# Kernel tuning notes

Hardware: AMD Instinct MI355X
Metric: run time of the kernel (lower is better)

The kernel has to match this reference:

```python
import jax, jax.numpy as jnp
import numpy as np

B, T, W, E, H, EMB, NVOCAB, WIN = 256, 200, 200, 768, 256, 32, 201, 8


def setup_inputs() -> dict:
    key = jax.random.key(0)
    ks = jax.random.split(key, 12)
    s = 0.05
    inputs = jax.random.normal(ks[0], (B, T, E), jnp.float32)
    full_word_embeddings = jax.random.normal(ks[1], (B, W, E), jnp.float32)
    lengths = jax.random.randint(ks[2], (B,), T // 2, T + 1)
    fix = jax.random.randint(ks[3], (B, T), 1, NVOCAB)
    fix_seq = jnp.where(jnp.arange(T)[None, :] < lengths[:, None], fix, 0)
    emb_table = (jax.random.normal(ks[4], (NVOCAB, EMB)) * s).at[0].set(0.0)  # padding_idx=0
    W_ih = jax.random.normal(ks[5], (3 * H, E + EMB)) * s  # torch GRU layout, gates r,z,n
    W_hh = jax.random.normal(ks[6], (3 * H, H)) * s
    b_ih = jax.random.normal(ks[7], (3 * H,)) * s
    b_hh = jax.random.normal(ks[8], (3 * H,)) * s
    W_out = jax.random.normal(ks[9], (E, H)) * s  # output_layer: Linear(H, E)
    b_out = jnp.zeros((E,), jnp.float32)
    W_dur = jax.random.normal(ks[10], (1, H)) * s  # duration_layer: Linear(H, 1)
    b_dur = jnp.zeros((1,), jnp.float32)
    return {"inputs": inputs, "fix_seq": fix_seq, "full_word_embeddings": full_word_embeddings,
            "lengths": lengths, "expert_id": 0, "emb_table": emb_table,
            "W_ih": W_ih, "b_ih": b_ih, "W_hh": W_hh, "b_hh": b_hh,
            "W_out": W_out, "b_out": b_out, "W_dur": W_dur, "b_dur": b_dur}


def _gru(x, W_ih, b_ih, W_hh, b_hh, h_dim):
    # x: [B,T,I]. Precompute input projections once, scan over time.
    xg = jnp.einsum('bti,gi->btg', x, W_ih) + b_ih  # [B,T,3H]

    def step(h, xg_t):
        hg = h @ W_hh.T + b_hh
        xr, xz, xn = jnp.split(xg_t, 3, axis=-1)
        hr, hz, hn = jnp.split(hg, 3, axis=-1)
        r = jax.nn.sigmoid(xr + hr)
        z = jax.nn.sigmoid(xz + hz)
        n = jnp.tanh(xn + r * hn)
        h_new = (1.0 - z) * n + z * h
        return h_new, h_new

    h0 = jnp.zeros((x.shape[0], h_dim), x.dtype)
    _, outs = jax.lax.scan(step, h0, jnp.swapaxes(xg, 0, 1))
    return jnp.swapaxes(outs, 0, 1)  # [B,T,H]


def reference(inputs, fix_seq, full_word_embeddings, lengths, expert_id,
              emb_table, W_ih, b_ih, W_hh, b_hh, W_out, b_out, W_dur, b_dur):
    del expert_id  # weights of the selected expert are passed directly
    valid_mask = fix_seq != 0
    scan_emb = emb_table[fix_seq]  # [B,T,32]
    rnn_in = jnp.concatenate([inputs, scan_emb], axis=-1)
    outputs = _gru(rnn_in, W_ih, b_ih, W_hh, b_hh, W_hh.shape[1])  # [B,T,H]
    # pad_packed_sequence zeros outputs beyond each sequence length
    tmask = jnp.arange(outputs.shape[1])[None, :] < lengths[:, None]
    outputs = outputs * tmask[..., None].astype(outputs.dtype)
    # dot attention: proj then scores against word embeddings
    proj = outputs @ W_out.T + b_out  # [B,T,E]
    logits = jnp.einsum('bte,bwe->btw', proj, full_word_embeddings)
    # saccade window mask around current fixation position
    wpos = jnp.arange(full_word_embeddings.shape[1])[None, None, :]
    dist = jnp.abs(wpos - fix_seq[..., None])
    sacc = (dist <= WIN) & valid_mask[..., None]
    logits = jnp.where(sacc, logits, -1e9)
    word_mask = jnp.sum(jnp.abs(full_word_embeddings), axis=-1) != 0
    logits = jnp.where(word_mask[:, None, :], logits, -1e9)
    dur_pred = (outputs @ W_dur.T + b_dur)[..., 0]  # [B,T]
    return logits, dur_pred
```

## Files before the change

kernel.cpp:

```cpp
#include <hip/hip_runtime.h>
#include <hip/hip_bf16.h>

typedef __attribute__((ext_vector_type(8))) short bf16x8;
typedef __attribute__((ext_vector_type(4))) float f32x4;
typedef __attribute__((ext_vector_type(4))) int   i32x4;

#define NB 256
#define NT 200
#define NW 200
#define NE 768
#define NH 256
#define NEMB 32
#define KIN 800
#define G3H 768
#define MROWS 51200

__device__ __forceinline__ float bf2f(unsigned short h) {
    return __uint_as_float(((unsigned)h) << 16);
}
__device__ __forceinline__ unsigned short f2bf(float f) {
    unsigned u = __float_as_uint(f);
    u += 0x7fff + ((u >> 16) & 1);
    return (unsigned short)(u >> 16);
}
__device__ __forceinline__ float sigm(float x) { return 1.0f / (1.0f + __expf(-x)); }
__device__ __forceinline__ float tanh_fast(float x) {
    float e = __expf(2.0f * x);
    return 1.0f - 2.0f / (e + 1.0f);
}

#if __has_builtin(__builtin_amdgcn_sdot4)
__device__ __forceinline__ int SDOT4(int a, int b, int c) {
    return __builtin_amdgcn_sdot4(a, b, c, false);
}
#else
__device__ __forceinline__ int SDOT4(int a, int b, int c) {
    #pragma unroll
    for (int j = 0; j < 4; j++)
        c += (int)(signed char)(a >> (8 * j)) * (int)(signed char)(b >> (8 * j));
    return c;
}
#endif

__device__ __forceinline__ void gload16(const void* g, void* l) {
    __builtin_amdgcn_global_load_lds((const __attribute__((address_space(1))) unsigned int*)g,
                                     (__attribute__((address_space(3))) unsigned int*)l,
                                     16, 0, 0);
}

__global__ void prep1(const float* __restrict__ inputs, const int* __restrict__ fix_seq,
                      const float* __restrict__ emb, const float* __restrict__ Wih,
                      const float* __restrict__ Wout, const float* __restrict__ bih,
                      const float* __restrict__ bhh,
                      unsigned short* __restrict__ Abf, unsigned short* __restrict__ Wihbf,
                      unsigned short* __restrict__ WoutTbf, float* __restrict__ biasC,
                      float* __restrict__ bias0) {
    const long gid0 = (long)blockIdx.x * blockDim.x + threadIdx.x;
    if (gid0 < G3H) biasC[gid0] = bih[gid0] + (gid0 < 512 ? bhh[gid0] : 0.0f);
    if (gid0 < NH) bias0[gid0] = 0.0f;
    const long NA = (long)MROWS * 100;
    const long NWU = 768L * 100;
    const long NOU = 256L * 96;
    const long total = NA + NWU + NOU;
    for (long u = gid0; u < total; u += (long)gridDim.x * blockDim.x) {
        bf16x8 v;
        unsigned short* dst;
        if (u < NA) {
            long row = u / 100;
            int c8 = (int)(u % 100) * 8;
            const float* s;
            if (c8 < NE) {
                s = inputs + row * NE + c8;
            } else {
                int fx = fix_seq[row];
                s = emb + (long)fx * NEMB + (c8 - NE);
            }
            #pragma unroll
            for (int j = 0; j < 8; j++) v[j] = (short)f2bf(s[j]);
            dst = Abf + row * KIN + c8;
        } else if (u < NA + NWU) {
            long u2 = u - NA;
            long row = u2 / 100;
            int c8 = (int)(u2 % 100) * 8;
            const float* s = Wih + row * KIN + c8;
            #pragma unroll
            for (int j = 0; j < 8; j++) v[j] = (short)f2bf(s[j]);
            dst = Wihbf + row * KIN + c8;
        } else {
            long u3 = u - NA - NWU;
            long row = u3 / 96;
            int c8 = (int)(u3 % 96) * 8;
            #pragma unroll
            for (int j = 0; j < 8; j++)
                v[j] = (short)f2bf(Wout[(long)(c8 + j) * NH + row]);
            dst = WoutTbf + row * NE + c8;
        }
        *(bf16x8*)dst = v;
    }
}

__global__ __launch_bounds__(256)
void gemm_bt128(const unsigned short* __restrict__ A,
                const unsigned short* __restrict__ Bw,
                const float* __restrict__ bias,
                unsigned short* __restrict__ Out,
                int M, int N, int K) {
    __shared__ unsigned short As[2][128 * 32];
    __shared__ unsigned short Bs[2][128 * 32];
    const int bid = (int)((blockIdx.x & 7) * (gridDim.x >> 3) + (blockIdx.x >> 3));
    const int nblk = N >> 7;
    const int m0 = (bid / nblk) << 7;
    const int n0 = (bid % nblk) << 7;
    const int tid = threadIdx.x;
    const int lane = tid & 63;
    const int wave = tid >> 6;
    const int wm = (wave >> 1) << 6;
    const int wn = (wave & 1) << 6;
    const int nk = K >> 5;

    const int srow = tid >> 2;
    const int sseg = (tid & 3) << 4;
    const char* gA0 = (const char*)(A + (long)(m0 + srow) * K) + sseg;
    const char* gA1 = (const char*)(A + (long)(m0 + 64 + srow) * K) + sseg;
    const char* gB0 = (const char*)(Bw + (long)(n0 + srow) * K) + sseg;
    const char* gB1 = (const char*)(Bw + (long)(n0 + 64 + srow) * K) + sseg;
    const int lofs = wave * 1024;

    f32x4 acc[4][4] = {};

    gload16(gA0, (char*)As[0] + lofs);
    gload16(gA1, (char*)As[0] + 4096 + lofs);
    gload16(gB0, (char*)Bs[0] + lofs);
    gload16(gB1, (char*)Bs[0] + 4096 + lofs);
    __syncthreads();

    int cur = 0;
    for (int kt = 0; kt < nk; kt++) {
        if (kt + 1 < nk) {
            gload16(gA0 + (kt + 1) * 64, (char*)As[cur ^ 1] + lofs);
            gload16(gA1 + (kt + 1) * 64, (char*)As[cur ^ 1] + 4096 + lofs);
            gload16(gB0 + (kt + 1) * 64, (char*)Bs[cur ^ 1] + lofs);
            gload16(gB1 + (kt + 1) * 64, (char*)Bs[cur ^ 1] + 4096 + lofs);
        }
        bf16x8 af[4], bfr[4];
        #pragma unroll
        for (int mi = 0; mi < 4; mi++)
            af[mi] = *(const bf16x8*)((const char*)As[cur] +
                        (wm + mi * 16 + (lane & 15)) * 64 + ((lane >> 4) << 4));
        #pragma unroll
        for (int ni = 0; ni < 4; ni++)
            bfr[ni] = *(const bf16x8*)((const char*)Bs[cur] +
                        (wn + ni * 16 + (lane & 15)) * 64 + ((lane >> 4) << 4));
        #pragma unroll
        for (int mi = 0; mi < 4; mi++)
            #pragma unroll
            for (int ni = 0; ni < 4; ni++)
                acc[mi][ni] = __builtin_amdgcn_mfma_f32_16x16x32_bf16(
                                  af[mi], bfr[ni], acc[mi][ni], 0, 0, 0);
        __syncthreads();
        cur ^= 1;
    }
    #pragma unroll
    for (int ni = 0; ni < 4; ni++) {
        const int col = n0 + wn + ni * 16 + (lane & 15);
        const float bv = bias[col];
        #pragma unroll
        for (int mi = 0; mi < 4; mi++) {
            const int row = m0 + wm + mi * 16 + ((lane >> 4) << 2);
            #pragma unroll
            for (int r = 0; r < 4; r++)
                Out[(long)(row + r) * N + col] = f2bf(acc[mi][ni][r] + bv);
        }
    }
}

__global__ __launch_bounds__(512, 2)
__attribute__((amdgpu_waves_per_eu(2, 2)))
void gru_scan(const unsigned short* __restrict__ xg,
              const float* __restrict__ Whh,
              const float* __restrict__ bhh,
              const int* __restrict__ lengths,
              unsigned short* __restrict__ hout) {
    __shared__ __align__(16) unsigned char h8[2][256];
    const int tid = threadIdx.x;
    const int lane = tid & 63;
    const int wave = tid >> 6;
    const int b = blockIdx.x;
    const int col = wave * 32 + (lane & 31);
    const int kh = lane >> 5;

    int W[3][32];
    #pragma unroll
    for (int g = 0; g < 3; g++) {
        const float* wr = Whh + (long)(g * 256 + col) * NH + kh * 128;
        #pragma unroll
        for (int d = 0; d < 32; d++) {
            const float4 f = *(const float4*)(wr + d * 4);
            unsigned pack = 0;
            #pragma unroll
            for (int j = 0; j < 4; j++) {
                const float fv = j == 0 ? f.x : j == 1 ? f.y : j == 2 ? f.z : f.w;
                int wq = (int)rintf(fv * 400.0f);
                wq = wq > 127 ? 127 : (wq < -127 ? -127 : wq);
                pack |= ((unsigned)(wq & 0xff)) << (8 * j);
            }
            W[g][d] = (int)pack;
        }
    }
    const float bhn = bhh[512 + col];
    const int len = lengths[b];
    if (tid < 128) ((unsigned*)h8)[tid] = 0u;

    const unsigned short* xrow = xg + (long)b * NT * G3H;
    unsigned short xv0 = xrow[col], xv1 = xrow[256 + col], xv2 = xrow[512 + col];
    float hp = 0.0f;
    const float ISC = 1.0f / (400.0f * 127.0f);
    const bool wlo = (lane < 32);

    asm volatile("s_waitcnt lgkmcnt(0)" ::: "memory");
    __builtin_amdgcn_sched_barrier(0);
    __builtin_amdgcn_s_barrier();
    __builtin_amdgcn_sched_barrier(0);

    for (int t = 0; t < NT; t++) {
        const unsigned char* hb = h8[(t + 1) & 1] + kh * 128;
        int p0a = 0, p0b = 0, p1a = 0, p1b = 0, p2a = 0, p2b = 0;
        #pragma unroll
        for (int r = 0; r < 8; r++) {
            const i32x4 hv = *(const i32x4*)(hb + r * 16);
            p0a = SDOT4(hv[0], W[0][r * 4 + 0], p0a);
            p1a = SDOT4(hv[0], W[1][r * 4 + 0], p1a);
            p2a = SDOT4(hv[0], W[2][r * 4 + 0], p2a);
            p0b = SDOT4(hv[1], W[0][r * 4 + 1], p0b);
            p1b = SDOT4(hv[1], W[1][r * 4 + 1], p1b);
            p2b = SDOT4(hv[1], W[2][r * 4 + 1], p2b);
            p0a = SDOT4(hv[2], W[0][r * 4 + 2], p0a);
            p1a = SDOT4(hv[2], W[1][r * 4 + 2], p1a);
            p2a = SDOT4(hv[2], W[2][r * 4 + 2], p2a);
            p0b = SDOT4(hv[3], W[0][r * 4 + 3], p0b);
            p1b = SDOT4(hv[3], W[1][r * 4 + 3], p1b);
            p2b = SDOT4(hv[3], W[2][r * 4 + 3], p2b);
        }
        int p0 = p0a + p0b, p1 = p1a + p1b, p2 = p2a + p2b;
        p0 += __shfl_xor(p0, 32);
        p1 += __shfl_xor(p1, 32);
        p2 += __shfl_xor(p2, 32);
        const float r = sigm(bf2f(xv0) + (float)p0 * ISC);
        const float z = sigm(bf2f(xv1) + (float)p1 * ISC);
        const float n = tanh_fast(bf2f(xv2) + r * ((float)p2 * ISC + bhn));
        hp = (1.0f - z) * n + z * hp;
        if (wlo) {
            h8[t & 1][col] = (unsigned char)((int)rintf(hp * 127.0f) & 0xff);
            hout[((long)b * NT + t) * NH + col] = (t < len) ? f2bf(hp) : (unsigned short)0;
        }
        if (t + 1 < NT) {
            const unsigned short* xn = xrow + (long)(t + 1) * G3H;
            xv0 = xn[col]; xv1 = xn[256 + col]; xv2 = xn[512 + col];
        }
        asm volatile("s_waitcnt lgkmcnt(0)" ::: "memory");
        __builtin_amdgcn_sched_barrier(0);
        __builtin_amdgcn_s_barrier();
        __builtin_amdgcn_sched_barrier(0);
    }
}

__global__ void prep2(const float* __restrict__ fwe, const float* __restrict__ bout,
                      unsigned short* __restrict__ fwebf,
                      unsigned char* __restrict__ wmask, float* __restrict__ dvec) {
    const int row = (int)((blockIdx.x * blockDim.x + threadIdx.x) >> 6);
    const int lane = threadIdx.x & 63;
    if (row >= MROWS) return;
    const float* s = fwe + (long)row * NE;
    unsigned short* d = fwebf + (long)row * NE;
    float asum = 0.0f, vdot = 0.0f;
    #pragma unroll
    for (int i = 0; i < 12; i++) {
        const float v = s[lane + i * 64];
        asum += fabsf(v);
        vdot += v * bout[lane + i * 64];
        d[lane + i * 64] = f2bf(v);
    }
    #pragma unroll
    for (int off = 32; off >= 1; off >>= 1) {
        asum += __shfl_xor(asum, off);
        vdot += __shfl_xor(vdot, off);
    }
    if (lane == 0) {
        wmask[row] = (asum != 0.0f) ? 1 : 0;
        dvec[row] = vdot;
    }
}

__global__ __launch_bounds__(256)
void logits_dur(const unsigned short* __restrict__ Hrow,
                const unsigned short* __restrict__ G,
                const int* __restrict__ fix_seq,
                const unsigned char* __restrict__ wmask,
                const float* __restrict__ dvec,
                const float* __restrict__ Wdur, const float* __restrict__ bdur,
                float* __restrict__ out) {
    __shared__ float dots[4][20];
    const int wv = threadIdx.x >> 6;
    const int gwave = (int)blockIdx.x * 4 + wv;
    const int lane = threadIdx.x & 63;
    const int l16 = lane & 15;
    const int grp = lane >> 4;
    const int b = gwave / NT;

    const unsigned short* hp = Hrow + (long)gwave * NH + l16 * 16;
    const bf16x8 h0 = *(const bf16x8*)hp;
    const bf16x8 h1 = *(const bf16x8*)(hp + 8);
    float hf[16];
    #pragma unroll
    for (int j = 0; j < 8; j++) { hf[j] = bf2f((unsigned short)h0[j]);
                                  hf[8 + j] = bf2f((unsigned short)h1[j]); }

    const int fix = fix_seq[gwave];
    const int wbase = fix - 8;

    if (fix != 0) {
        #pragma unroll
        for (int it = 0; it < 5; it++) {
            const int wi = it * 4 + grp;
            int w = wbase + wi;
            w = w < 0 ? 0 : (w > NW - 1 ? NW - 1 : w);
            const unsigned short* gp = G + ((long)b * NW + w) * NH + l16 * 16;
            const bf16x8 g0 = *(const bf16x8*)gp;
            const bf16x8 g1 = *(const bf16x8*)(gp + 8);
            float p = 0.0f;
            #pragma unroll
            for (int j = 0; j < 8; j++) {
                p += hf[j] * bf2f((unsigned short)g0[j]);
                p += hf[8 + j] * bf2f((unsigned short)g1[j]);
            }
            p += __shfl_xor(p, 1); p += __shfl_xor(p, 2);
            p += __shfl_xor(p, 4); p += __shfl_xor(p, 8);
            if (l16 == 0 && wi < 17) dots[wv][wi] = p;
        }
    }
    float pd = 0.0f;
    #pragma unroll
    for (int j = 0; j < 16; j++) pd += hf[j] * Wdur[l16 * 16 + j];
    pd += __shfl_xor(pd, 1); pd += __shfl_xor(pd, 2);
    pd += __shfl_xor(pd, 4); pd += __shfl_xor(pd, 8);
    if (lane == 0) out[(long)NB * NT * NW + gwave] = pd + bdur[0];

    __syncthreads();

    if (lane < 50) {
        float4 o;
        #pragma unroll
        for (int c = 0; c < 4; c++) {
            const int w = lane * 4 + c;
            const int wi = w - wbase;
            const int wic = wi < 0 ? 0 : (wi > 16 ? 16 : wi);
            const bool ok = (fix != 0) && ((unsigned)wi < 17u) && (wmask[b * NW + w] != 0);
            const float val = dots[wv][wic] + dvec[b * NW + w];
            ((float*)&o)[c] = ok ? val : -1e9f;
        }
        *(float4*)(out + (long)gwave * NW + lane * 4) = o;
    }
}

extern "C" void kernel_launch(void* const* d_in, const int* in_sizes, int n_in,
                              void* d_out, int out_size, void* d_ws, size_t ws_size,
                              hipStream_t stream) {
    (void)in_sizes; (void)n_in; (void)out_size; (void)ws_size;
    const float* inputs  = (const float*)d_in[0];
    const int*   fix_seq = (const int*)d_in[1];
    const float* fwe     = (const float*)d_in[2];
    const int*   lengths = (const int*)d_in[3];
    const float* emb     = (const float*)d_in[5];
    const float* Wih     = (const float*)d_in[6];
    const float* bih     = (const float*)d_in[7];
    const float* Whh     = (const float*)d_in[8];
    const float* bhh     = (const float*)d_in[9];
    const float* Wout    = (const float*)d_in[10];
    const float* bout    = (const float*)d_in[11];
    const float* Wdur    = (const float*)d_in[12];
    const float* bdur    = (const float*)d_in[13];
    float* out = (float*)d_out;

    char* ws = (char*)d_ws;
    unsigned short* Abf     = (unsigned short*)(ws);
    unsigned short* xgbf    = (unsigned short*)(ws + 81920000);
    unsigned short* hout    = (unsigned short*)(ws + 160563200);
    unsigned short* Wihbf   = (unsigned short*)(ws + 186777600);
    unsigned short* WoutTbf = (unsigned short*)(ws + 188006400);
    unsigned char*  wmask   = (unsigned char*)(ws + 188399616);
    float*          biasC   = (float*)(ws + 188450816);
    float*          dvec    = (float*)(ws + 188453888);
    float*          bias0   = (float*)(ws + 188658688);
    unsigned short* fwebf   = Abf;
    unsigned short* Gbf     = xgbf;

    prep1<<<2048, 256, 0, stream>>>(inputs, fix_seq, emb, Wih, Wout, bih, bhh,
                                    Abf, Wihbf, WoutTbf, biasC, bias0);
    gemm_bt128<<<400 * 6, 256, 0, stream>>>(Abf, Wihbf, biasC, xgbf, MROWS, G3H, KIN);
    prep2<<<12800, 256, 0, stream>>>(fwe, bout, fwebf, wmask, dvec);
    gru_scan<<<256, 512, 0, stream>>>(xgbf, Whh, bhh, lengths, hout);
    gemm_bt128<<<400 * 2, 256, 0, stream>>>(fwebf, WoutTbf, bias0, Gbf, MROWS, NH, NE);
    logits_dur<<<12800, 256, 0, stream>>>(hout, Gbf, fix_seq, wmask, dvec, Wdur, bdur, out);
}
```

Measured before the change: 508.6 us.

## Overlap the word-embedding projection GEMM with the GRU scan in one launch

Extra blocks are added to the GRU scan kernel. Blocks past the batch count compute the fwe·W_out^T GEMM tile by tile, so that work runs on CUs left idle by the 256 latency-bound scan blocks. G is written to a separate workspace region, because xgbf is still being read by the scan. The fused path requires a larger workspace and falls back to the old two-kernel path otherwise. The in-kernel GEMM uses a simpler unpipelined load loop and raises shared memory per block, which may reduce scan-block occupancy or contend for bandwidth.

```diff
diff --git a/kernel.cpp b/kernel.cpp
--- a/kernel.cpp
+++ b/kernel.cpp
@@ -176,15 +176,91 @@
 
 __global__ __launch_bounds__(512, 2)
 __attribute__((amdgpu_waves_per_eu(2, 2)))
-void gru_scan(const unsigned short* __restrict__ xg,
-              const float* __restrict__ Whh,
-              const float* __restrict__ bhh,
-              const int* __restrict__ lengths,
-              unsigned short* __restrict__ hout) {
-    __shared__ __align__(16) unsigned char h8[2][256];
+void gru_fused(const unsigned short* __restrict__ xg,
+               const float* __restrict__ Whh,
+               const float* __restrict__ bhh,
+               const int* __restrict__ lengths,
+               unsigned short* __restrict__ hout,
+               const unsigned short* __restrict__ Afw,
+               const unsigned short* __restrict__ BwT,
+               unsigned short* __restrict__ G) {
+    __shared__ __align__(16) char smem[512 + 2 * 16384];
     const int tid = threadIdx.x;
     const int lane = tid & 63;
     const int wave = tid >> 6;
+
+    if (blockIdx.x >= NB) {
+        const int roleblk = (int)blockIdx.x - NB;
+        const int sub = tid >> 8;
+        const int tid4 = tid & 255;
+        const int wave4 = tid4 >> 6;
+        const int srow = tid4 >> 2;
+        const int sseg = (tid4 & 3) << 4;
+        char* base = smem + 512 + sub * 16384;
+        char* lA0 = base + wave4 * 1024;
+        char* lA1 = base + 4096 + wave4 * 1024;
+        char* lB0 = base + 8192 + wave4 * 1024;
+        char* lB1 = base + 12288 + wave4 * 1024;
+        const int wm = (wave4 >> 1) << 6;
+        const int wn = (wave4 & 1) << 6;
+
+        for (int round = 0; round < 2; round++) {
+            const int tile = roleblk * 2 + sub + round * 512;
+            const bool active = tile < 800;
+            const int tc = active ? tile : 0;
+            const int m0 = (tc >> 1) << 7;
+            const int n0 = (tc & 1) << 7;
+            const char* gA0 = (const char*)(Afw + (long)(m0 + srow) * NE) + sseg;
+            const char* gA1 = (const char*)(Afw + (long)(m0 + 64 + srow) * NE) + sseg;
+            const char* gB0 = (const char*)(BwT + (long)(n0 + srow) * NE) + sseg;
+            const char* gB1 = (const char*)(BwT + (long)(n0 + 64 + srow) * NE) + sseg;
+            f32x4 acc[4][4] = {};
+            for (int kt = 0; kt < 24; kt++) {
+                __syncthreads();
+                if (active) {
+                    gload16(gA0 + kt * 64, lA0);
+                    gload16(gA1 + kt * 64, lA1);
+                    gload16(gB0 + kt * 64, lB0);
+                    gload16(gB1 + kt * 64, lB1);
+                    asm volatile("s_waitcnt vmcnt(0)" ::: "memory");
+                }
+                __syncthreads();
+                if (active) {
+                    bf16x8 af[4], bfr[4];
+                    #pragma unroll
+                    for (int mi = 0; mi < 4; mi++)
+                        af[mi] = *(const bf16x8*)(base +
+                                    (wm + mi * 16 + (lane & 15)) * 64 + ((lane >> 4) << 4));
+                    #pragma unroll
+                    for (int ni = 0; ni < 4; ni++)
+                        bfr[ni] = *(const bf16x8*)(base + 8192 +
+                                    (wn + ni * 16 + (lane & 15)) * 64 + ((lane >> 4) << 4));
+                    #pragma unroll
+                    for (int mi = 0; mi < 4; mi++)
+                        #pragma unroll
+                        for (int ni = 0; ni < 4; ni++)
+                            acc[mi][ni] = __builtin_amdgcn_mfma_f32_16x16x32_bf16(
+                                              af[mi], bfr[ni], acc[mi][ni], 0, 0, 0);
+                }
+            }
+            if (active) {
+                #pragma unroll
+                for (int ni = 0; ni < 4; ni++) {
+                    const int col = n0 + wn + ni * 16 + (lane & 15);
+                    #pragma unroll
+                    for (int mi = 0; mi < 4; mi++) {
+                        const int row = m0 + wm + mi * 16 + ((lane >> 4) << 2);
+                        #pragma unroll
+                        for (int r = 0; r < 4; r++)
+                            G[(long)(row + r) * NH + col] = f2bf(acc[mi][ni][r]);
+                    }
+                }
+            }
+        }
+        return;
+    }
+
+    unsigned char (*h8)[256] = (unsigned char (*)[256])smem;
     const int b = blockIdx.x;
     const int col = wave * 32 + (lane & 31);
     const int kh = lane >> 5;
@@ -365,7 +441,7 @@
 extern "C" void kernel_launch(void* const* d_in, const int* in_sizes, int n_in,
                               void* d_out, int out_size, void* d_ws, size_t ws_size,
                               hipStream_t stream) {
-    (void)in_sizes; (void)n_in; (void)out_size; (void)ws_size;
+    (void)in_sizes; (void)n_in; (void)out_size;
     const float* inputs  = (const float*)d_in[0];
     const int*   fix_seq = (const int*)d_in[1];
     const float* fwe     = (const float*)d_in[2];
@@ -392,13 +468,23 @@
     float*          dvec    = (float*)(ws + 188453888);
     float*          bias0   = (float*)(ws + 188658688);
     unsigned short* fwebf   = Abf;
-    unsigned short* Gbf     = xgbf;
+
+    const bool fused = (ws_size >= 214874112ull);
+    unsigned short* Gbf = fused ? (unsigned short*)(ws + 188659712)
+                                : xgbf;
 
     prep1<<<2048, 256, 0, stream>>>(inputs, fix_seq, emb, Wih, Wout, bih, bhh,
                                     Abf, Wihbf, WoutTbf, biasC, bias0);
     gemm_bt128<<<400 * 6, 256, 0, stream>>>(Abf, Wihbf, biasC, xgbf, MROWS, G3H, KIN);
     prep2<<<12800, 256, 0, stream>>>(fwe, bout, fwebf, wmask, dvec);
-    gru_scan<<<256, 512, 0, stream>>>(xgbf, Whh, bhh, lengths, hout);
-    gemm_bt128<<<400 * 2, 256, 0, stream>>>(fwebf, WoutTbf, bias0, Gbf, MROWS, NH, NE);
+    if (fused) {
+        gru_fused<<<512, 512, 0, stream>>>(xgbf, Whh, bhh, lengths, hout,
+                                           fwebf, WoutTbf, Gbf);
+    } else {
+        gru_fused<<<256, 512, 0, stream>>>(xgbf, Whh, bhh, lengths, hout,
+                                           fwebf, WoutTbf, Gbf);
+        gemm_bt128<<<400 * 2, 256, 0, stream>>>(fwebf, WoutTbf, bias0, Gbf,
+                                                MROWS, NH, NE);
+    }
     logits_dur<<<12800, 256, 0, stream>>>(hout, Gbf, fix_seq, wmask, dvec, Wdur, bdur, out);
 }
```

After: 518.9 us. 1.02x slower.

## Fuse fp32-to-bf16 conversion and row stats of word embeddings into G GEMM

Applied to the files above, without the earlier changes.

Replaces the separate prep2 conversion pass and the bf16 GEMM for G with one GEMM kernel. It loads fp32 word embeddings directly, converts them to bf16 into LDS, and computes the abs-sum mask and bias dot-products along the way. This removes the intermediate bf16 copy's write and re-read and one kernel launch. In exchange, each row tile's fp32 data is read by both column-tile blocks, and the new kernel does not overlap loads with MFMA work.

```diff
diff --git a/kernel.cpp b/kernel.cpp
--- a/kernel.cpp
+++ b/kernel.cpp
@@ -53,11 +53,9 @@
                       const float* __restrict__ Wout, const float* __restrict__ bih,
                       const float* __restrict__ bhh,
                       unsigned short* __restrict__ Abf, unsigned short* __restrict__ Wihbf,
-                      unsigned short* __restrict__ WoutTbf, float* __restrict__ biasC,
-                      float* __restrict__ bias0) {
+                      unsigned short* __restrict__ WoutTbf, float* __restrict__ biasC) {
     const long gid0 = (long)blockIdx.x * blockDim.x + threadIdx.x;
     if (gid0 < G3H) biasC[gid0] = bih[gid0] + (gid0 < 512 ? bhh[gid0] : 0.0f);
-    if (gid0 < NH) bias0[gid0] = 0.0f;
     const long NA = (long)MROWS * 100;
     const long NWU = 768L * 100;
     const long NOU = 256L * 96;
@@ -174,6 +172,121 @@
     }
 }
 
+__global__ __launch_bounds__(256)
+void gemmG_f32(const float* __restrict__ fwe,
+               const unsigned short* __restrict__ BwT,
+               const float* __restrict__ bout,
+               unsigned short* __restrict__ G,
+               unsigned char* __restrict__ wmask,
+               float* __restrict__ dvec) {
+    __shared__ unsigned short As[128 * 32];
+    __shared__ unsigned short Bs[128 * 32];
+    __shared__ float Bo[G3H];
+    const int bid = (int)((blockIdx.x & 7) * (gridDim.x >> 3) + (blockIdx.x >> 3));
+    const int m0 = (bid >> 1) << 7;
+    const int n0 = (bid & 1) << 7;
+    const int tid = threadIdx.x;
+    const int lane = tid & 63;
+    const int wave = tid >> 6;
+    const int wm = (wave >> 1) << 6;
+    const int wn = (wave & 1) << 6;
+
+    const int srow = tid >> 2;
+    const int sseg = (tid & 3) << 4;
+    const char* gB0 = (const char*)(BwT + (long)(n0 + srow) * NE) + sseg;
+    const char* gB1 = (const char*)(BwT + (long)(n0 + 64 + srow) * NE) + sseg;
+    char* lB0 = (char*)Bs + wave * 1024;
+    char* lB1 = (char*)Bs + 4096 + wave * 1024;
+
+    const int arow = tid >> 1;
+    const int akh = tid & 1;
+    const float* aptr = fwe + (long)(m0 + arow) * NE + akh * 16;
+    char* la = (char*)As + arow * 64 + akh * 32;
+
+    for (int i = tid; i < G3H; i += 256) Bo[i] = bout[i];
+
+    float4 fa0 = *(const float4*)(aptr);
+    float4 fa1 = *(const float4*)(aptr + 4);
+    float4 fa2 = *(const float4*)(aptr + 8);
+    float4 fa3 = *(const float4*)(aptr + 12);
+
+    f32x4 acc[4][4] = {};
+    float asum = 0.0f, vdot = 0.0f;
+
+    __syncthreads();
+
+    for (int kt = 0; kt < 24; kt++) {
+        __syncthreads();
+        gload16(gB0 + kt * 64, lB0);
+        gload16(gB1 + kt * 64, lB1);
+        const float* bo = Bo + kt * 32 + akh * 16;
+        const float4 b0 = *(const float4*)(bo);
+        const float4 b1 = *(const float4*)(bo + 4);
+        const float4 b2 = *(const float4*)(bo + 8);
+        const float4 b3 = *(const float4*)(bo + 12);
+        asum += fabsf(fa0.x) + fabsf(fa0.y) + fabsf(fa0.z) + fabsf(fa0.w)
+              + fabsf(fa1.x) + fabsf(fa1.y) + fabsf(fa1.z) + fabsf(fa1.w)
+              + fabsf(fa2.x) + fabsf(fa2.y) + fabsf(fa2.z) + fabsf(fa2.w)
+              + fabsf(fa3.x) + fabsf(fa3.y) + fabsf(fa3.z) + fabsf(fa3.w);
+        vdot += fa0.x * b0.x + fa0.y * b0.y + fa0.z * b0.z + fa0.w * b0.w
+              + fa1.x * b1.x + fa1.y * b1.y + fa1.z * b1.z + fa1.w * b1.w
+              + fa2.x * b2.x + fa2.y * b2.y + fa2.z * b2.z + fa2.w * b2.w
+              + fa3.x * b3.x + fa3.y * b3.y + fa3.z * b3.z + fa3.w * b3.w;
+        bf16x8 v0, v1;
+        v0[0] = (short)f2bf(fa0.x); v0[1] = (short)f2bf(fa0.y);
+        v0[2] = (short)f2bf(fa0.z); v0[3] = (short)f2bf(fa0.w);
+        v0[4] = (short)f2bf(fa1.x); v0[5] = (short)f2bf(fa1.y);
+        v0[6] = (short)f2bf(fa1.z); v0[7] = (short)f2bf(fa1.w);
+        v1[0] = (short)f2bf(fa2.x); v1[1] = (short)f2bf(fa2.y);
+        v1[2] = (short)f2bf(fa2.z); v1[3] = (short)f2bf(fa2.w);
+        v1[4] = (short)f2bf(fa3.x); v1[5] = (short)f2bf(fa3.y);
+        v1[6] = (short)f2bf(fa3.z); v1[7] = (short)f2bf(fa3.w);
+        *(bf16x8*)la = v0;
+        *(bf16x8*)(la + 16) = v1;
+        asm volatile("s_waitcnt vmcnt(0)" ::: "memory");
+        __syncthreads();
+        if (kt + 1 < 24) {
+            const float* ap = aptr + (kt + 1) * 32;
+            fa0 = *(const float4*)(ap);
+            fa1 = *(const float4*)(ap + 4);
+            fa2 = *(const float4*)(ap + 8);
+            fa3 = *(const float4*)(ap + 12);
+        }
+        bf16x8 af[4], bfr[4];
+        #pragma unroll
+        for (int mi = 0; mi < 4; mi++)
+            af[mi] = *(const bf16x8*)((const char*)As +
+                        (wm + mi * 16 + (lane & 15)) * 64 + ((lane >> 4) << 4));
+        #pragma unroll
+        for (int ni = 0; ni < 4; ni++)
+            bfr[ni] = *(const bf16x8*)((const char*)Bs +
+                        (wn + ni * 16 + (lane & 15)) * 64 + ((lane >> 4) << 4));
+        #pragma unroll
+        for (int mi = 0; mi < 4; mi++)
+            #pragma unroll
+            for (int ni = 0; ni < 4; ni++)
+                acc[mi][ni] = __builtin_amdgcn_mfma_f32_16x16x32_bf16(
+                                  af[mi], bfr[ni], acc[mi][ni], 0, 0, 0);
+    }
+    asum += __shfl_xor(asum, 1);
+    vdot += __shfl_xor(vdot, 1);
+    if (akh == 0) {
+        wmask[m0 + arow] = (asum != 0.0f) ? 1 : 0;
+        dvec[m0 + arow] = vdot;
+    }
+    #pragma unroll
+    for (int ni = 0; ni < 4; ni++) {
+        const int col = n0 + wn + ni * 16 + (lane & 15);
+        #pragma unroll
+        for (int mi = 0; mi < 4; mi++) {
+            const int row = m0 + wm + mi * 16 + ((lane >> 4) << 2);
+            #pragma unroll
+            for (int r = 0; r < 4; r++)
+                G[(long)(row + r) * NH + col] = f2bf(acc[mi][ni][r]);
+        }
+    }
+}
+
 __global__ __launch_bounds__(512, 2)
 __attribute__((amdgpu_waves_per_eu(2, 2)))
 void gru_scan(const unsigned short* __restrict__ xg,
@@ -261,33 +374,6 @@
         __builtin_amdgcn_sched_barrier(0);
         __builtin_amdgcn_s_barrier();
         __builtin_amdgcn_sched_barrier(0);
-    }
-}
-
-__global__ void prep2(const float* __restrict__ fwe, const float* __restrict__ bout,
-                      unsigned short* __restrict__ fwebf,
-                      unsigned char* __restrict__ wmask, float* __restrict__ dvec) {
-    const int row = (int)((blockIdx.x * blockDim.x + threadIdx.x) >> 6);
-    const int lane = threadIdx.x & 63;
-    if (row >= MROWS) return;
-    const float* s = fwe + (long)row * NE;
-    unsigned short* d = fwebf + (long)row * NE;
-    float asum = 0.0f, vdot = 0.0f;
-    #pragma unroll
-    for (int i = 0; i < 12; i++) {
-        const float v = s[lane + i * 64];
-        asum += fabsf(v);
-        vdot += v * bout[lane + i * 64];
-        d[lane + i * 64] = f2bf(v);
-    }
-    #pragma unroll
-    for (int off = 32; off >= 1; off >>= 1) {
-        asum += __shfl_xor(asum, off);
-        vdot += __shfl_xor(vdot, off);
-    }
-    if (lane == 0) {
-        wmask[row] = (asum != 0.0f) ? 1 : 0;
-        dvec[row] = vdot;
     }
 }
 
@@ -390,15 +476,12 @@
     unsigned char*  wmask   = (unsigned char*)(ws + 188399616);
     float*          biasC   = (float*)(ws + 188450816);
     float*          dvec    = (float*)(ws + 188453888);
-    float*          bias0   = (float*)(ws + 188658688);
-    unsigned short* fwebf   = Abf;
-    unsigned short* Gbf     = xgbf;
+    unsigned short* Gbf     = Abf;
 
     prep1<<<2048, 256, 0, stream>>>(inputs, fix_seq, emb, Wih, Wout, bih, bhh,
-                                    Abf, Wihbf, WoutTbf, biasC, bias0);
+                                    Abf, Wihbf, WoutTbf, biasC);
     gemm_bt128<<<400 * 6, 256, 0, stream>>>(Abf, Wihbf, biasC, xgbf, MROWS, G3H, KIN);
-    prep2<<<12800, 256, 0, stream>>>(fwe, bout, fwebf, wmask, dvec);
+    gemmG_f32<<<800, 256, 0, stream>>>(fwe, WoutTbf, bout, Gbf, wmask, dvec);
     gru_scan<<<256, 512, 0, stream>>>(xgbf, Whh, bhh, lengths, hout);
-    gemm_bt128<<<400 * 2, 256, 0, stream>>>(fwebf, WoutTbf, bias0, Gbf, MROWS, NH, NE);
     logits_dur<<<12800, 256, 0, stream>>>(hout, Gbf, fix_seq, wmask, dvec, Wdur, bdur, out);
 }
```

New measurement: 501.2 us. About the same (-1.5%).
